# Optimization experiments

Measured on AMD Instinct MI355X. Metric: run time of the kernel, lower is better.

Reference implementation:

```python
import jax, jax.numpy as jnp
import numpy as np

B, S, D = 4, 2048, 512
H, DK, DV = 8, 64, 64
DFF = 2048
LN_EPS = 1e-5


def _layernorm(x, g, b):
    mu = jnp.mean(x, axis=-1, keepdims=True)
    var = jnp.mean(jnp.square(x - mu), axis=-1, keepdims=True)
    return (x - mu) * jax.lax.rsqrt(var + LN_EPS) * g + b


def setup_inputs() -> dict:
    key = jax.random.key(0)
    ks = jax.random.split(key, 9)
    def xavier(k, shape):
        fan_out, fan_in = shape
        std = np.sqrt(2.0 / (fan_in + fan_out))
        return jax.random.normal(k, shape, jnp.float32) * std
    GELU_GAIN = 1.85
    return {
        "x": jax.random.normal(ks[0], (B, S, D), jnp.float32),
        "attention_mask": jax.random.randint(ks[1], (B, S), 0, 2).astype(bool),
        "Wq": xavier(ks[2], (H * DK, D)),
        "Wk": xavier(ks[3], (H * DK, D)),
        "Wv": xavier(ks[4], (H * DV, D)),
        "Wp": xavier(ks[5], (D, H * DV)),
        "W1": xavier(ks[6], (DFF, D)) * GELU_GAIN,
        "b1": jnp.zeros((DFF,), jnp.float32),
        "W2": xavier(ks[7], (D, DFF)),
        "b2": jnp.zeros((D,), jnp.float32),
        "ln1_g": jnp.ones((D,), jnp.float32),
        "ln1_b": jnp.zeros((D,), jnp.float32),
        "ln2_g": jnp.ones((D,), jnp.float32),
        "ln2_b": jnp.zeros((D,), jnp.float32),
    }


def reference(x, attention_mask, Wq, Wk, Wv, Wp, W1, b1, W2, b2,
              ln1_g, ln1_b, ln2_g, ln2_b):
    b, s, d = x.shape
    residual = x
    q = (x @ Wq.T).reshape(b, s, H, DK)  # [B,S,H,DK]
    k = (x @ Wk.T).reshape(b, s, H, DK)
    v = (x @ Wv.T).reshape(b, s, H, DV)
    score = jnp.einsum("bshd,bthd->bhst", q, k) * (DK ** -0.5)  # [B,H,S,S]
    # subtractive mask: score -= 100 * not(mask)
    score = score - 100.0 * (~attention_mask)[:, None, None, :].astype(score.dtype)
    p = jax.nn.softmax(score, axis=-1)
    ctx = jnp.einsum("bhst,bthd->bshd", p, v).reshape(b, s, H * DV)
    att = ctx @ Wp.T  # dropout p=0.1 is identity in eval
    h = _layernorm(att + residual, ln1_g, ln1_b)
    ff = jax.nn.gelu(h @ W1.T + b1, approximate=False) @ W2.T + b2
    out = _layernorm(ff + h, ln2_g, ln2_b)
    return out
```

## Files before the change

kernel.cpp:

```cpp
#include <hip/hip_runtime.h>
#include <cstdint>
#include <cstddef>

#define B_ 4
#define S_ 2048
#define D_ 512
#define H_ 8
#define DK_ 64
#define DFF_ 2048

using s16x8  = __attribute__((ext_vector_type(8))) short;
using bf16x8 = __attribute__((ext_vector_type(8))) __bf16;
using f32x4  = __attribute__((ext_vector_type(4))) float;

__device__ __forceinline__ short f2bf(float f) {
  unsigned u = __builtin_bit_cast(unsigned, f);
  u += 0x7FFFu + ((u >> 16) & 1u);
  return (short)(u >> 16);
}
__device__ __forceinline__ float bf2f(short s) {
  unsigned u = ((unsigned)(unsigned short)s) << 16;
  return __builtin_bit_cast(float, u);
}

__device__ __forceinline__ void gl2lds16(const void* g, void* l) {
  __builtin_amdgcn_global_load_lds(
      (const __attribute__((address_space(1))) void*)g,
      (__attribute__((address_space(3))) void*)l, 16, 0, 0);
}

__global__ __launch_bounds__(256)
void cvt_all(const float* __restrict__ x, const float* __restrict__ Wq,
             const float* __restrict__ Wk, const float* __restrict__ Wv,
             const float* __restrict__ Wp, const float* __restrict__ W1,
             const float* __restrict__ W2,
             short* __restrict__ xb, short* __restrict__ wqkv,
             short* __restrict__ wp, short* __restrict__ w1, short* __restrict__ w2) {
  int blk = blockIdx.x;
  const float* src; short* dst; int off;
  if (blk < 4096)      { src = x;  dst = xb;            off = blk; }
  else if (blk < 4352) { src = Wq; dst = wqkv;          off = blk - 4096; }
  else if (blk < 4608) { src = Wk; dst = wqkv + 262144; off = blk - 4352; }
  else if (blk < 4864) { src = Wv; dst = wqkv + 524288; off = blk - 4608; }
  else if (blk < 5120) { src = Wp; dst = wp;            off = blk - 4864; }
  else if (blk < 6144) { src = W1; dst = w1;            off = blk - 5120; }
  else                 { src = W2; dst = w2;            off = blk - 6144; }
  int i = (off * 256 + threadIdx.x) * 4;
  float4 v = *(const float4*)(src + i);
  *(short4*)(dst + i) = make_short4(f2bf(v.x), f2bf(v.y), f2bf(v.z), f2bf(v.w));
}

__global__ __launch_bounds__(256) void mask_detect(const unsigned* __restrict__ m,
                                                   unsigned* __restrict__ flag) {
  int i = blockIdx.x * 256 + threadIdx.x;
  unsigned v = m[i];
  if (v) atomicOr(flag, v);
}

__global__ __launch_bounds__(256) void mask_convert(const void* __restrict__ m,
                                                    const unsigned* __restrict__ flag,
                                                    float* __restrict__ mb) {
  int i = blockIdx.x * 256 + threadIdx.x;
  unsigned f = *flag;
  int v;
  if ((f & ~1u) == 0u)            v = ((const int*)m)[i];
  else if (f == 0x3F800000u)      v = (((const float*)m)[i] != 0.0f);
  else                            v = ((const unsigned char*)m)[i];
  mb[i] = v ? 0.0f : -100.0f;
}

constexpr int BM = 128, BN = 128, BK = 32;

template <int MODE>
__global__ __launch_bounds__(256)
void gemm_bt(const short* __restrict__ A, const short* __restrict__ B,
             int M, int N, int K,
             const float* __restrict__ aux1,
             void* __restrict__ out0, void* __restrict__ out1, void* __restrict__ out2) {
  __shared__ alignas(16) short As[BM][BK];
  __shared__ alignas(16) short Bs[BN][BK];

  const int tid  = threadIdx.x;
  const int lane = tid & 63;
  const int wave = tid >> 6;
  const int quad = lane >> 4;
  const int l16  = lane & 15;
  const int wm   = (wave >> 1) * 64;
  const int wn   = (wave & 1) * 64;
  const int bm   = blockIdx.x * BM;
  const int bn   = blockIdx.y * BN;

  const short* Ag = A + (size_t)(bm + wave * 32 + (lane >> 2)) * K + (lane & 3) * 8;
  const short* Bg = B + (size_t)(bn + wave * 32 + (lane >> 2)) * K + (lane & 3) * 8;
  short* AsW = &As[wave * 32][0];
  short* BsW = &Bs[wave * 32][0];
  const size_t row16 = (size_t)16 * K;

  f32x4 acc[4][4] = {};

  for (int k0 = 0; k0 < K; k0 += BK) {
    gl2lds16(Ag + k0,          AsW);
    gl2lds16(Ag + k0 + row16,  AsW + 16 * BK);
    gl2lds16(Bg + k0,          BsW);
    gl2lds16(Bg + k0 + row16,  BsW + 16 * BK);
    __syncthreads();

    bf16x8 a[4], b[4];
#pragma unroll
    for (int i = 0; i < 4; ++i)
      a[i] = __builtin_bit_cast(bf16x8, *(const s16x8*)&As[wm + i * 16 + l16][quad * 8]);
#pragma unroll
    for (int j = 0; j < 4; ++j)
      b[j] = __builtin_bit_cast(bf16x8, *(const s16x8*)&Bs[wn + j * 16 + l16][quad * 8]);
#pragma unroll
    for (int i = 0; i < 4; ++i)
#pragma unroll
      for (int j = 0; j < 4; ++j)
        acc[i][j] = __builtin_amdgcn_mfma_f32_16x16x32_bf16(a[i], b[j], acc[i][j], 0, 0, 0);
    __syncthreads();
  }

#pragma unroll
  for (int i = 0; i < 4; ++i) {
    const int m0 = bm + wm + i * 16 + quad * 4;
#pragma unroll
    for (int j = 0; j < 4; ++j) {
      const int n = bn + wn + j * 16 + l16;
      if constexpr (MODE == 0) {
        const int bb = m0 >> 11, ss0 = m0 & 2047;
        if (n >= 1024) {
          const int nn = n - 1024;
          short4 pk = make_short4(f2bf(acc[i][j][0]), f2bf(acc[i][j][1]),
                                  f2bf(acc[i][j][2]), f2bf(acc[i][j][3]));
          *(short4*)((short*)out2 +
              ((((size_t)bb * H_ + (nn >> 6)) * 64 + (nn & 63)) * S_ + ss0)) = pk;
        } else {
          short* dst = (n < 512) ? (short*)out0 : (short*)out1;
          const float sc_ = (n < 512) ? 0.125f : 1.0f;
          const int hh = (n >> 6) & 7, dd = n & 63;
          const size_t rowb = ((size_t)bb * H_ + hh) * S_ + ss0;
#pragma unroll
          for (int rr = 0; rr < 4; ++rr)
            dst[(rowb + rr) * 64 + dd] = f2bf(acc[i][j][rr] * sc_);
        }
      } else {
#pragma unroll
        for (int rr = 0; rr < 4; ++rr) {
          float t = acc[i][j][rr] + aux1[n];
          float gl = 0.5f * t * (1.0f + erff(t * 0.70710678118f));
          ((short*)out0)[(size_t)(m0 + rr) * N + n] = f2bf(gl);
        }
      }
    }
  }
}

template <int MODE>
__global__ __launch_bounds__(128)
void gemm_bt2(const short* __restrict__ A, const short* __restrict__ B,
              int M, int N, int K,
              const float* __restrict__ aux1, const short* __restrict__ auxb,
              float* __restrict__ out0) {
  __shared__ alignas(16) short As[128][32];
  __shared__ alignas(16) short Bs[64][32];

  const int tid  = threadIdx.x;
  const int lane = tid & 63;
  const int wave = tid >> 6;
  const int quad = lane >> 4;
  const int l16  = lane & 15;
  const int wm   = wave * 64;
  const int bm   = blockIdx.x * 128;
  const int bn   = blockIdx.y * 64;

  const int srow = wave * 16 + (lane >> 2);
  const int scol = (lane & 3) * 8;
  const short* Ag = A + (size_t)(bm + srow) * K + scol;
  const short* Bg = B + (size_t)(bn + srow) * K + scol;
  short* AsW = &As[wave * 16][0];
  short* BsW = &Bs[wave * 16][0];
  const size_t row32 = (size_t)32 * K;

  f32x4 acc[4][4] = {};

  for (int k0 = 0; k0 < K; k0 += 32) {
    gl2lds16(Ag + k0,              AsW);
    gl2lds16(Ag + k0 + row32,      AsW + 32 * 32);
    gl2lds16(Ag + k0 + 2 * row32,  AsW + 64 * 32);
    gl2lds16(Ag + k0 + 3 * row32,  AsW + 96 * 32);
    gl2lds16(Bg + k0,              BsW);
    gl2lds16(Bg + k0 + row32,      BsW + 32 * 32);
    __syncthreads();

    bf16x8 a[4], b[4];
#pragma unroll
    for (int i = 0; i < 4; ++i)
      a[i] = __builtin_bit_cast(bf16x8, *(const s16x8*)&As[wm + i * 16 + l16][quad * 8]);
#pragma unroll
    for (int j = 0; j < 4; ++j)
      b[j] = __builtin_bit_cast(bf16x8, *(const s16x8*)&Bs[j * 16 + l16][quad * 8]);
#pragma unroll
    for (int i = 0; i < 4; ++i)
#pragma unroll
      for (int j = 0; j < 4; ++j)
        acc[i][j] = __builtin_amdgcn_mfma_f32_16x16x32_bf16(a[i], b[j], acc[i][j], 0, 0, 0);
    __syncthreads();
  }

#pragma unroll
  for (int i = 0; i < 4; ++i) {
    const int m0 = bm + wm + i * 16 + quad * 4;
#pragma unroll
    for (int j = 0; j < 4; ++j) {
      const int n = bn + j * 16 + l16;
#pragma unroll
      for (int rr = 0; rr < 4; ++rr) {
        float v = acc[i][j][rr];
        if constexpr (MODE == 1) {
          out0[(size_t)(m0 + rr) * N + n] = v + aux1[(size_t)(m0 + rr) * N + n];
        } else {
          out0[(size_t)(m0 + rr) * N + n] =
              v + aux1[n] + bf2f(auxb[(size_t)(m0 + rr) * N + n]);
        }
      }
    }
  }
}

__global__ __launch_bounds__(256)
void flash_attn_mfma(const short* __restrict__ Qb, const short* __restrict__ Kb,
                     const short* __restrict__ Vtg, const float* __restrict__ maskbias,
                     short* __restrict__ ctxb) {
  __shared__ alignas(16) short Ks[64][72];
  __shared__ alignas(16) short Vt[64][72];
  __shared__ alignas(16) short Ps[4][32][72];
  __shared__ alignas(16) float mrow[S_];

  const int b = blockIdx.z, h = blockIdx.y;
  const int tid = threadIdx.x;
  const int w = tid >> 6, lane = tid & 63;
  const int quad = lane >> 4, l16 = lane & 15;
  const size_t base  = ((size_t)(b * H_ + h)) * S_ * DK_;
  const size_t baseT = ((size_t)(b * H_ + h)) * DK_ * S_;
  const int q0 = blockIdx.x * 128;

  {
    const float4* mp = (const float4*)(maskbias + (size_t)b * S_);
    ((float4*)mrow)[tid]       = mp[tid];
    ((float4*)mrow)[tid + 256] = mp[tid + 256];
  }

  bf16x8 qa[2][2];
#pragma unroll
  for (int st = 0; st < 2; ++st) {
    const short* qp = Qb + base + (size_t)(q0 + w * 32 + st * 16 + l16) * 64 + quad * 8;
    qa[st][0] = __builtin_bit_cast(bf16x8, *(const s16x8*)(qp));
    qa[st][1] = __builtin_bit_cast(bf16x8, *(const s16x8*)(qp + 32));
  }

  f32x4 Oc[2][4] = {};
  float li[2][4] = {};

  const int r = tid >> 2, c16 = (tid & 3) * 16;
  const short* kp = Kb  + base  + (size_t)r * 64 + c16;
  const short* vp = Vtg + baseT + (size_t)r * S_ + c16;

  s16x8 kr0 = *(const s16x8*)(kp);
  s16x8 kr1 = *(const s16x8*)(kp + 8);
  s16x8 vr0 = *(const s16x8*)(vp);
  s16x8 vr1 = *(const s16x8*)(vp + 8);

  for (int t0 = 0; t0 < S_; t0 += 64) {
    __syncthreads();
    *(s16x8*)&Ks[r][c16]     = kr0;
    *(s16x8*)&Ks[r][c16 + 8] = kr1;
    *(s16x8*)&Vt[r][c16]     = vr0;
    *(s16x8*)&Vt[r][c16 + 8] = vr1;
    __syncthreads();

    if (t0 + 64 < S_) {
      kr0 = *(const s16x8*)(kp + (size_t)(t0 + 64) * 64);
      kr1 = *(const s16x8*)(kp + (size_t)(t0 + 64) * 64 + 8);
      vr0 = *(const s16x8*)(vp + t0 + 64);
      vr1 = *(const s16x8*)(vp + t0 + 64 + 8);
    }

    f32x4 sc[2][4] = {};
#pragma unroll
    for (int c = 0; c < 2; ++c) {
#pragma unroll
      for (int jt = 0; jt < 4; ++jt) {
        bf16x8 kb = __builtin_bit_cast(bf16x8,
            *(const s16x8*)&Ks[jt * 16 + l16][c * 32 + quad * 8]);
        sc[0][jt] = __builtin_amdgcn_mfma_f32_16x16x32_bf16(qa[0][c], kb, sc[0][jt], 0, 0, 0);
        sc[1][jt] = __builtin_amdgcn_mfma_f32_16x16x32_bf16(qa[1][c], kb, sc[1][jt], 0, 0, 0);
      }
    }

    float mb4[4];
#pragma unroll
    for (int jt = 0; jt < 4; ++jt) mb4[jt] = mrow[t0 + jt * 16 + l16];
#pragma unroll
    for (int st = 0; st < 2; ++st) {
#pragma unroll
      for (int jt = 0; jt < 4; ++jt) {
#pragma unroll
        for (int rr = 0; rr < 4; ++rr) {
          float p = __expf(sc[st][jt][rr] + mb4[jt]);
          unsigned u = __builtin_bit_cast(unsigned, p) & 0xFFFF0000u;
          li[st][rr] += __builtin_bit_cast(float, u);
          Ps[w][st * 16 + quad * 4 + rr][jt * 16 + l16] = (short)(u >> 16);
        }
      }
    }

#pragma unroll
    for (int c = 0; c < 2; ++c) {
      bf16x8 pa0 = __builtin_bit_cast(bf16x8,
          *(const s16x8*)&Ps[w][l16][c * 32 + quad * 8]);
      bf16x8 pa1 = __builtin_bit_cast(bf16x8,
          *(const s16x8*)&Ps[w][16 + l16][c * 32 + quad * 8]);
#pragma unroll
      for (int dt = 0; dt < 4; ++dt) {
        bf16x8 vb = __builtin_bit_cast(bf16x8,
            *(const s16x8*)&Vt[dt * 16 + l16][c * 32 + quad * 8]);
        Oc[0][dt] = __builtin_amdgcn_mfma_f32_16x16x32_bf16(pa0, vb, Oc[0][dt], 0, 0, 0);
        Oc[1][dt] = __builtin_amdgcn_mfma_f32_16x16x32_bf16(pa1, vb, Oc[1][dt], 0, 0, 0);
      }
    }
  }

#pragma unroll
  for (int st = 0; st < 2; ++st) {
#pragma unroll
    for (int rr = 0; rr < 4; ++rr) {
      float l = li[st][rr];
#pragma unroll
      for (int m = 1; m < 16; m <<= 1) l += __shfl_xor(l, m);
      float inv = 1.f / l;
      const size_t row = (size_t)b * S_ + q0 + w * 32 + st * 16 + quad * 4 + rr;
#pragma unroll
      for (int dt = 0; dt < 4; ++dt)
        ctxb[row * (H_ * DK_) + h * 64 + dt * 16 + l16] = f2bf(Oc[st][dt][rr] * inv);
    }
  }
}

__global__ __launch_bounds__(256)
void ln_kernel(const float* __restrict__ y, const float* __restrict__ g,
               const float* __restrict__ bb, float* __restrict__ out32,
               short* __restrict__ outb) {
  const int wave = threadIdx.x >> 6, lane = threadIdx.x & 63;
  const int token = blockIdx.x * 4 + wave;
  const float* row = y + (size_t)token * D_;
  float4 v0 = *(const float4*)(row + lane * 8);
  float4 v1 = *(const float4*)(row + lane * 8 + 4);
  float sum = v0.x + v0.y + v0.z + v0.w + v1.x + v1.y + v1.z + v1.w;
#pragma unroll
  for (int m = 1; m < 64; m <<= 1) sum += __shfl_xor(sum, m);
  float mu = sum * (1.0f / D_);
  float d0 = v0.x - mu, d1 = v0.y - mu, d2 = v0.z - mu, d3 = v0.w - mu;
  float d4 = v1.x - mu, d5 = v1.y - mu, d6 = v1.z - mu, d7 = v1.w - mu;
  float vs = d0*d0 + d1*d1 + d2*d2 + d3*d3 + d4*d4 + d5*d5 + d6*d6 + d7*d7;
#pragma unroll
  for (int m = 1; m < 64; m <<= 1) vs += __shfl_xor(vs, m);
  float rstd = rsqrtf(vs * (1.0f / D_) + 1e-5f);
  float o[8] = {d0, d1, d2, d3, d4, d5, d6, d7};
  int c = lane * 8;
#pragma unroll
  for (int i = 0; i < 8; ++i) {
    float val = o[i] * rstd * g[c + i] + bb[c + i];
    if (out32) out32[(size_t)token * D_ + c + i] = val;
    if (outb)  outb[(size_t)token * D_ + c + i] = f2bf(val);
  }
}

constexpr size_t OFF_XB   = 0;
constexpr size_t OFF_WQKV = 8388608;
constexpr size_t OFF_WP   = 9961472;
constexpr size_t OFF_W1   = 10485760;
constexpr size_t OFF_W2   = 12582912;
constexpr size_t OFF_Q    = 14680064;
constexpr size_t OFF_K    = 23068672;
constexpr size_t OFF_VT   = 31457280;
constexpr size_t OFF_CTX  = 39845888;
constexpr size_t OFF_Y1   = 48234496;
constexpr size_t OFF_HB   = 81788928;
constexpr size_t OFF_FF1  = 14680064;
constexpr size_t OFF_Y2   = 48234496;
constexpr size_t OFF_MB   = 90177536;
constexpr size_t OFF_FLAG = 90210304;
constexpr size_t WS_NEED  = 90210308;

extern "C" void kernel_launch(void* const* d_in, const int* in_sizes, int n_in,
                              void* d_out, int out_size, void* d_ws, size_t ws_size,
                              hipStream_t stream) {
  if (ws_size < WS_NEED) return;

  const float* x    = (const float*)d_in[0];
  const void*  msk  = d_in[1];
  const float* Wq   = (const float*)d_in[2];
  const float* Wk   = (const float*)d_in[3];
  const float* Wv   = (const float*)d_in[4];
  const float* Wp   = (const float*)d_in[5];
  const float* W1   = (const float*)d_in[6];
  const float* b1   = (const float*)d_in[7];
  const float* W2   = (const float*)d_in[8];
  const float* b2   = (const float*)d_in[9];
  const float* ln1g = (const float*)d_in[10];
  const float* ln1b = (const float*)d_in[11];
  const float* ln2g = (const float*)d_in[12];
  const float* ln2b = (const float*)d_in[13];

  char* ws = (char*)d_ws;
  short* xb    = (short*)(ws + OFF_XB);
  short* wqkv  = (short*)(ws + OFF_WQKV);
  short* Wpb   = (short*)(ws + OFF_WP);
  short* W1b   = (short*)(ws + OFF_W1);
  short* W2b   = (short*)(ws + OFF_W2);
  short* Qbh   = (short*)(ws + OFF_Q);
  short* Kbh   = (short*)(ws + OFF_K);
  short* VTb   = (short*)(ws + OFF_VT);
  short* ctxb  = (short*)(ws + OFF_CTX);
  float* y1    = (float*)(ws + OFF_Y1);
  short* hb    = (short*)(ws + OFF_HB);
  short* ff1b  = (short*)(ws + OFF_FF1);
  float* y2    = (float*)(ws + OFF_Y2);
  float* mbias = (float*)(ws + OFF_MB);
  unsigned* flag = (unsigned*)(ws + OFF_FLAG);

  hipMemsetAsync(flag, 0, 4, stream);
  mask_detect<<<8, 256, 0, stream>>>((const unsigned*)msk, flag);
  mask_convert<<<32, 256, 0, stream>>>(msk, flag, mbias);

  cvt_all<<<7168, 256, 0, stream>>>(x, Wq, Wk, Wv, Wp, W1, W2,
                                    xb, wqkv, Wpb, W1b, W2b);

  gemm_bt<0><<<dim3(64, 12), 256, 0, stream>>>(xb, wqkv, 8192, 1536, 512,
                                               nullptr, Qbh, Kbh, VTb);

  flash_attn_mfma<<<dim3(S_ / 128, H_, B_), 256, 0, stream>>>(Qbh, Kbh, VTb, mbias, ctxb);

  gemm_bt2<1><<<dim3(64, 8), 128, 0, stream>>>(ctxb, Wpb, 8192, 512, 512,
                                               x, nullptr, y1);

  ln_kernel<<<2048, 256, 0, stream>>>(y1, ln1g, ln1b, nullptr, hb);

  gemm_bt<2><<<dim3(64, 16), 256, 0, stream>>>(hb, W1b, 8192, 2048, 512,
                                               b1, ff1b, nullptr, nullptr);

  gemm_bt2<3><<<dim3(64, 8), 128, 0, stream>>>(ff1b, W2b, 8192, 512, 2048,
                                               b2, hb, y2);

  ln_kernel<<<2048, 256, 0, stream>>>(y2, ln2g, ln2b, (float*)d_out, nullptr);
}
```

Measured before the change: 342.6 us.

## Use 2-wave attention blocks with 64 query rows per wave, store Q transposed

The flash attention kernel now runs 128 threads per block, and each wave handles 64 query rows instead of 32. Each K/V tile loaded into shared memory is therefore reused across more MFMAs per wave, and staging moves to 4 vectors per thread. The QKV GEMM epilogue now writes Q transposed with packed short4 stores (same layout as V), and the attention kernel gathers Q with scalar strided loads. This adds register pressure (launch bounds 128,1), halves the waves per block, and makes the one-time Q load uncoalesced.

```diff
diff --git a/kernel.cpp b/kernel.cpp
--- a/kernel.cpp
+++ b/kernel.cpp
@@ -128,20 +128,24 @@
       const int n = bn + wn + j * 16 + l16;
       if constexpr (MODE == 0) {
         const int bb = m0 >> 11, ss0 = m0 & 2047;
-        if (n >= 1024) {
+        if (n < 512) {
+          short4 pk = make_short4(f2bf(acc[i][j][0] * 0.125f), f2bf(acc[i][j][1] * 0.125f),
+                                  f2bf(acc[i][j][2] * 0.125f), f2bf(acc[i][j][3] * 0.125f));
+          *(short4*)((short*)out0 +
+              ((((size_t)bb * H_ + (n >> 6)) * 64 + (n & 63)) * S_ + ss0)) = pk;
+        } else if (n >= 1024) {
           const int nn = n - 1024;
           short4 pk = make_short4(f2bf(acc[i][j][0]), f2bf(acc[i][j][1]),
                                   f2bf(acc[i][j][2]), f2bf(acc[i][j][3]));
           *(short4*)((short*)out2 +
               ((((size_t)bb * H_ + (nn >> 6)) * 64 + (nn & 63)) * S_ + ss0)) = pk;
         } else {
-          short* dst = (n < 512) ? (short*)out0 : (short*)out1;
-          const float sc_ = (n < 512) ? 0.125f : 1.0f;
-          const int hh = (n >> 6) & 7, dd = n & 63;
+          const int nn = n - 512;
+          const int hh = nn >> 6, dd = nn & 63;
           const size_t rowb = ((size_t)bb * H_ + hh) * S_ + ss0;
 #pragma unroll
           for (int rr = 0; rr < 4; ++rr)
-            dst[(rowb + rr) * 64 + dd] = f2bf(acc[i][j][rr] * sc_);
+            ((short*)out1)[(rowb + rr) * 64 + dd] = f2bf(acc[i][j][rr]);
         }
       } else {
 #pragma unroll
@@ -227,13 +231,13 @@
   }
 }
 
-__global__ __launch_bounds__(256)
-void flash_attn_mfma(const short* __restrict__ Qb, const short* __restrict__ Kb,
+__global__ __launch_bounds__(128, 1)
+void flash_attn_mfma(const short* __restrict__ QTg, const short* __restrict__ Kb,
                      const short* __restrict__ Vtg, const float* __restrict__ maskbias,
                      short* __restrict__ ctxb) {
   __shared__ alignas(16) short Ks[64][72];
   __shared__ alignas(16) short Vt[64][72];
-  __shared__ alignas(16) short Ps[4][32][72];
+  __shared__ alignas(16) short Ps[2][64][72];
   __shared__ alignas(16) float mrow[S_];
 
   const int b = blockIdx.z, h = blockIdx.y;
@@ -246,54 +250,65 @@
 
   {
     const float4* mp = (const float4*)(maskbias + (size_t)b * S_);
-    ((float4*)mrow)[tid]       = mp[tid];
-    ((float4*)mrow)[tid + 256] = mp[tid + 256];
-  }
-
-  bf16x8 qa[2][2];
-#pragma unroll
-  for (int st = 0; st < 2; ++st) {
-    const short* qp = Qb + base + (size_t)(q0 + w * 32 + st * 16 + l16) * 64 + quad * 8;
-    qa[st][0] = __builtin_bit_cast(bf16x8, *(const s16x8*)(qp));
-    qa[st][1] = __builtin_bit_cast(bf16x8, *(const s16x8*)(qp + 32));
-  }
-
-  f32x4 Oc[2][4] = {};
-  float li[2][4] = {};
-
-  const int r = tid >> 2, c16 = (tid & 3) * 16;
-  const short* kp = Kb  + base  + (size_t)r * 64 + c16;
-  const short* vp = Vtg + baseT + (size_t)r * S_ + c16;
-
-  s16x8 kr0 = *(const s16x8*)(kp);
-  s16x8 kr1 = *(const s16x8*)(kp + 8);
-  s16x8 vr0 = *(const s16x8*)(vp);
-  s16x8 vr1 = *(const s16x8*)(vp + 8);
+#pragma unroll
+    for (int i = 0; i < 4; ++i) ((float4*)mrow)[tid + i * 128] = mp[tid + i * 128];
+  }
+
+  bf16x8 qa[4][2];
+#pragma unroll
+  for (int st = 0; st < 4; ++st) {
+    const int q = q0 + w * 64 + st * 16 + l16;
+#pragma unroll
+    for (int c = 0; c < 2; ++c) {
+      s16x8 t;
+#pragma unroll
+      for (int j = 0; j < 8; ++j)
+        t[j] = QTg[baseT + (size_t)(c * 32 + quad * 8 + j) * S_ + q];
+      qa[st][c] = __builtin_bit_cast(bf16x8, t);
+    }
+  }
+
+  f32x4 Oc[4][4] = {};
+  float li[4][4] = {};
+
+  const int r = tid >> 1, c32 = (tid & 1) * 32;
+  const short* kp = Kb  + base  + (size_t)r * 64 + c32;
+  const short* vp = Vtg + baseT + (size_t)r * S_ + c32;
+
+  s16x8 kr[4], vr[4];
+#pragma unroll
+  for (int u = 0; u < 4; ++u) {
+    kr[u] = *(const s16x8*)(kp + u * 8);
+    vr[u] = *(const s16x8*)(vp + u * 8);
+  }
 
   for (int t0 = 0; t0 < S_; t0 += 64) {
     __syncthreads();
-    *(s16x8*)&Ks[r][c16]     = kr0;
-    *(s16x8*)&Ks[r][c16 + 8] = kr1;
-    *(s16x8*)&Vt[r][c16]     = vr0;
-    *(s16x8*)&Vt[r][c16 + 8] = vr1;
+#pragma unroll
+    for (int u = 0; u < 4; ++u) {
+      *(s16x8*)&Ks[r][c32 + u * 8] = kr[u];
+      *(s16x8*)&Vt[r][c32 + u * 8] = vr[u];
+    }
     __syncthreads();
 
     if (t0 + 64 < S_) {
-      kr0 = *(const s16x8*)(kp + (size_t)(t0 + 64) * 64);
-      kr1 = *(const s16x8*)(kp + (size_t)(t0 + 64) * 64 + 8);
-      vr0 = *(const s16x8*)(vp + t0 + 64);
-      vr1 = *(const s16x8*)(vp + t0 + 64 + 8);
-    }
-
-    f32x4 sc[2][4] = {};
+#pragma unroll
+      for (int u = 0; u < 4; ++u) {
+        kr[u] = *(const s16x8*)(kp + (size_t)(t0 + 64) * 64 + u * 8);
+        vr[u] = *(const s16x8*)(vp + (t0 + 64) + u * 8);
+      }
+    }
+
+    f32x4 sc[4][4] = {};
 #pragma unroll
     for (int c = 0; c < 2; ++c) {
 #pragma unroll
       for (int jt = 0; jt < 4; ++jt) {
         bf16x8 kb = __builtin_bit_cast(bf16x8,
             *(const s16x8*)&Ks[jt * 16 + l16][c * 32 + quad * 8]);
-        sc[0][jt] = __builtin_amdgcn_mfma_f32_16x16x32_bf16(qa[0][c], kb, sc[0][jt], 0, 0, 0);
-        sc[1][jt] = __builtin_amdgcn_mfma_f32_16x16x32_bf16(qa[1][c], kb, sc[1][jt], 0, 0, 0);
+#pragma unroll
+        for (int st = 0; st < 4; ++st)
+          sc[st][jt] = __builtin_amdgcn_mfma_f32_16x16x32_bf16(qa[st][c], kb, sc[st][jt], 0, 0, 0);
       }
     }
 
@@ -301,7 +316,7 @@
 #pragma unroll
     for (int jt = 0; jt < 4; ++jt) mb4[jt] = mrow[t0 + jt * 16 + l16];
 #pragma unroll
-    for (int st = 0; st < 2; ++st) {
+    for (int st = 0; st < 4; ++st) {
 #pragma unroll
       for (int jt = 0; jt < 4; ++jt) {
 #pragma unroll
@@ -316,29 +331,31 @@
 
 #pragma unroll
     for (int c = 0; c < 2; ++c) {
-      bf16x8 pa0 = __builtin_bit_cast(bf16x8,
-          *(const s16x8*)&Ps[w][l16][c * 32 + quad * 8]);
-      bf16x8 pa1 = __builtin_bit_cast(bf16x8,
-          *(const s16x8*)&Ps[w][16 + l16][c * 32 + quad * 8]);
+      bf16x8 pa[4];
+#pragma unroll
+      for (int st = 0; st < 4; ++st)
+        pa[st] = __builtin_bit_cast(bf16x8,
+            *(const s16x8*)&Ps[w][st * 16 + l16][c * 32 + quad * 8]);
 #pragma unroll
       for (int dt = 0; dt < 4; ++dt) {
         bf16x8 vb = __builtin_bit_cast(bf16x8,
             *(const s16x8*)&Vt[dt * 16 + l16][c * 32 + quad * 8]);
-        Oc[0][dt] = __builtin_amdgcn_mfma_f32_16x16x32_bf16(pa0, vb, Oc[0][dt], 0, 0, 0);
-        Oc[1][dt] = __builtin_amdgcn_mfma_f32_16x16x32_bf16(pa1, vb, Oc[1][dt], 0, 0, 0);
-      }
-    }
-  }
-
-#pragma unroll
-  for (int st = 0; st < 2; ++st) {
+#pragma unroll
+        for (int st = 0; st < 4; ++st)
+          Oc[st][dt] = __builtin_amdgcn_mfma_f32_16x16x32_bf16(pa[st], vb, Oc[st][dt], 0, 0, 0);
+      }
+    }
+  }
+
+#pragma unroll
+  for (int st = 0; st < 4; ++st) {
 #pragma unroll
     for (int rr = 0; rr < 4; ++rr) {
       float l = li[st][rr];
 #pragma unroll
       for (int m = 1; m < 16; m <<= 1) l += __shfl_xor(l, m);
       float inv = 1.f / l;
-      const size_t row = (size_t)b * S_ + q0 + w * 32 + st * 16 + quad * 4 + rr;
+      const size_t row = (size_t)b * S_ + q0 + w * 64 + st * 16 + quad * 4 + rr;
 #pragma unroll
       for (int dt = 0; dt < 4; ++dt)
         ctxb[row * (H_ * DK_) + h * 64 + dt * 16 + l16] = f2bf(Oc[st][dt][rr] * inv);
@@ -380,7 +397,7 @@
 constexpr size_t OFF_WP   = 9961472;
 constexpr size_t OFF_W1   = 10485760;
 constexpr size_t OFF_W2   = 12582912;
-constexpr size_t OFF_Q    = 14680064;
+constexpr size_t OFF_QT   = 14680064;
 constexpr size_t OFF_K    = 23068672;
 constexpr size_t OFF_VT   = 31457280;
 constexpr size_t OFF_CTX  = 39845888;
@@ -418,7 +435,7 @@
   short* Wpb   = (short*)(ws + OFF_WP);
   short* W1b   = (short*)(ws + OFF_W1);
   short* W2b   = (short*)(ws + OFF_W2);
-  short* Qbh   = (short*)(ws + OFF_Q);
+  short* QTb   = (short*)(ws + OFF_QT);
   short* Kbh   = (short*)(ws + OFF_K);
   short* VTb   = (short*)(ws + OFF_VT);
   short* ctxb  = (short*)(ws + OFF_CTX);
@@ -437,9 +454,9 @@
                                     xb, wqkv, Wpb, W1b, W2b);
 
   gemm_bt<0><<<dim3(64, 12), 256, 0, stream>>>(xb, wqkv, 8192, 1536, 512,
-                                               nullptr, Qbh, Kbh, VTb);
-
-  flash_attn_mfma<<<dim3(S_ / 128, H_, B_), 256, 0, stream>>>(Qbh, Kbh, VTb, mbias, ctxb);
+                                               nullptr, QTb, Kbh, VTb);
+
+  flash_attn_mfma<<<dim3(S_ / 128, H_, B_), 128, 0, stream>>>(QTb, Kbh, VTb, mbias, ctxb);
 
   gemm_bt2<1><<<dim3(64, 8), 128, 0, stream>>>(ctxb, Wpb, 8192, 512, 512,
                                                x, nullptr, y1);
```

After: 347.9 us. No clear change (+1.5%).

## Split-K the N=512 GEMMs and fuse residual/bias adds into layernorm

Applied to the files above, without the earlier changes.

The two 512-wide output GEMMs now run with split-K over two z-slices, each writing raw fp32 partials. A fused layernorm kernel sums the partials and adds the residual (x or h) and bias before normalizing. This doubles the block count for the small-N GEMMs to fill more CUs, at the cost of extra fp32 partial traffic. Q is also stored transposed (d-major), like K-side V, so the QKV epilogue writes packed short4 stores, while flash attention gathers Q with strided scalar loads.

```diff
diff --git a/kernel.cpp b/kernel.cpp
--- a/kernel.cpp
+++ b/kernel.cpp
@@ -128,20 +128,24 @@
       const int n = bn + wn + j * 16 + l16;
       if constexpr (MODE == 0) {
         const int bb = m0 >> 11, ss0 = m0 & 2047;
-        if (n >= 1024) {
+        if (n < 512) {
+          short4 pk = make_short4(f2bf(acc[i][j][0] * 0.125f), f2bf(acc[i][j][1] * 0.125f),
+                                  f2bf(acc[i][j][2] * 0.125f), f2bf(acc[i][j][3] * 0.125f));
+          *(short4*)((short*)out0 +
+              ((((size_t)bb * H_ + (n >> 6)) * 64 + (n & 63)) * S_ + ss0)) = pk;
+        } else if (n >= 1024) {
           const int nn = n - 1024;
           short4 pk = make_short4(f2bf(acc[i][j][0]), f2bf(acc[i][j][1]),
                                   f2bf(acc[i][j][2]), f2bf(acc[i][j][3]));
           *(short4*)((short*)out2 +
               ((((size_t)bb * H_ + (nn >> 6)) * 64 + (nn & 63)) * S_ + ss0)) = pk;
         } else {
-          short* dst = (n < 512) ? (short*)out0 : (short*)out1;
-          const float sc_ = (n < 512) ? 0.125f : 1.0f;
-          const int hh = (n >> 6) & 7, dd = n & 63;
+          const int nn = n - 512;
+          const int hh = nn >> 6, dd = nn & 63;
           const size_t rowb = ((size_t)bb * H_ + hh) * S_ + ss0;
 #pragma unroll
           for (int rr = 0; rr < 4; ++rr)
-            dst[(rowb + rr) * 64 + dd] = f2bf(acc[i][j][rr] * sc_);
+            ((short*)out1)[(rowb + rr) * 64 + dd] = f2bf(acc[i][j][rr]);
         }
       } else {
 #pragma unroll
@@ -155,12 +159,9 @@
   }
 }
 
-template <int MODE>
 __global__ __launch_bounds__(128)
-void gemm_bt2(const short* __restrict__ A, const short* __restrict__ B,
-              int M, int N, int K,
-              const float* __restrict__ aux1, const short* __restrict__ auxb,
-              float* __restrict__ out0) {
+void gemm_bt2_sk(const short* __restrict__ A, const short* __restrict__ B,
+                 int M, int N, int K, float* __restrict__ outp) {
   __shared__ alignas(16) short As[128][32];
   __shared__ alignas(16) short Bs[64][32];
 
@@ -172,18 +173,20 @@
   const int wm   = wave * 64;
   const int bm   = blockIdx.x * 128;
   const int bn   = blockIdx.y * 64;
+  const int Kh   = K >> 1;
+  const int koff = blockIdx.z * Kh;
 
   const int srow = wave * 16 + (lane >> 2);
   const int scol = (lane & 3) * 8;
-  const short* Ag = A + (size_t)(bm + srow) * K + scol;
-  const short* Bg = B + (size_t)(bn + srow) * K + scol;
+  const short* Ag = A + (size_t)(bm + srow) * K + koff + scol;
+  const short* Bg = B + (size_t)(bn + srow) * K + koff + scol;
   short* AsW = &As[wave * 16][0];
   short* BsW = &Bs[wave * 16][0];
   const size_t row32 = (size_t)32 * K;
 
   f32x4 acc[4][4] = {};
 
-  for (int k0 = 0; k0 < K; k0 += 32) {
+  for (int k0 = 0; k0 < Kh; k0 += 32) {
     gl2lds16(Ag + k0,              AsW);
     gl2lds16(Ag + k0 + row32,      AsW + 32 * 32);
     gl2lds16(Ag + k0 + 2 * row32,  AsW + 64 * 32);
@@ -207,6 +210,7 @@
     __syncthreads();
   }
 
+  float* dst = outp + (size_t)blockIdx.z * M * N;
 #pragma unroll
   for (int i = 0; i < 4; ++i) {
     const int m0 = bm + wm + i * 16 + quad * 4;
@@ -214,21 +218,14 @@
     for (int j = 0; j < 4; ++j) {
       const int n = bn + j * 16 + l16;
 #pragma unroll
-      for (int rr = 0; rr < 4; ++rr) {
-        float v = acc[i][j][rr];
-        if constexpr (MODE == 1) {
-          out0[(size_t)(m0 + rr) * N + n] = v + aux1[(size_t)(m0 + rr) * N + n];
-        } else {
-          out0[(size_t)(m0 + rr) * N + n] =
-              v + aux1[n] + bf2f(auxb[(size_t)(m0 + rr) * N + n]);
-        }
-      }
+      for (int rr = 0; rr < 4; ++rr)
+        dst[(size_t)(m0 + rr) * N + n] = acc[i][j][rr];
     }
   }
 }
 
 __global__ __launch_bounds__(256)
-void flash_attn_mfma(const short* __restrict__ Qb, const short* __restrict__ Kb,
+void flash_attn_mfma(const short* __restrict__ QTg, const short* __restrict__ Kb,
                      const short* __restrict__ Vtg, const float* __restrict__ maskbias,
                      short* __restrict__ ctxb) {
   __shared__ alignas(16) short Ks[64][72];
@@ -253,9 +250,15 @@
   bf16x8 qa[2][2];
 #pragma unroll
   for (int st = 0; st < 2; ++st) {
-    const short* qp = Qb + base + (size_t)(q0 + w * 32 + st * 16 + l16) * 64 + quad * 8;
-    qa[st][0] = __builtin_bit_cast(bf16x8, *(const s16x8*)(qp));
-    qa[st][1] = __builtin_bit_cast(bf16x8, *(const s16x8*)(qp + 32));
+    const int q = q0 + w * 32 + st * 16 + l16;
+#pragma unroll
+    for (int c = 0; c < 2; ++c) {
+      s16x8 t;
+#pragma unroll
+      for (int j = 0; j < 8; ++j)
+        t[j] = QTg[baseT + (size_t)(c * 32 + quad * 8 + j) * S_ + q];
+      qa[st][c] = __builtin_bit_cast(bf16x8, t);
+    }
   }
 
   f32x4 Oc[2][4] = {};
@@ -347,31 +350,61 @@
 }
 
 __global__ __launch_bounds__(256)
-void ln_kernel(const float* __restrict__ y, const float* __restrict__ g,
-               const float* __restrict__ bb, float* __restrict__ out32,
-               short* __restrict__ outb) {
+void ln_fused(const float* __restrict__ p0, const float* __restrict__ p1,
+              const float* __restrict__ xres, const short* __restrict__ hres,
+              const float* __restrict__ bias,
+              const float* __restrict__ g, const float* __restrict__ bb,
+              float* __restrict__ out32, short* __restrict__ outb) {
   const int wave = threadIdx.x >> 6, lane = threadIdx.x & 63;
   const int token = blockIdx.x * 4 + wave;
-  const float* row = y + (size_t)token * D_;
-  float4 v0 = *(const float4*)(row + lane * 8);
-  float4 v1 = *(const float4*)(row + lane * 8 + 4);
-  float sum = v0.x + v0.y + v0.z + v0.w + v1.x + v1.y + v1.z + v1.w;
+  const size_t off = (size_t)token * D_;
+  const int c = lane * 8;
+
+  float v[8];
+  {
+    float4 a0 = *(const float4*)(p0 + off + c);
+    float4 a1 = *(const float4*)(p0 + off + c + 4);
+    float4 b0 = *(const float4*)(p1 + off + c);
+    float4 b1 = *(const float4*)(p1 + off + c + 4);
+    v[0]=a0.x+b0.x; v[1]=a0.y+b0.y; v[2]=a0.z+b0.z; v[3]=a0.w+b0.w;
+    v[4]=a1.x+b1.x; v[5]=a1.y+b1.y; v[6]=a1.z+b1.z; v[7]=a1.w+b1.w;
+  }
+  if (xres) {
+    float4 x0 = *(const float4*)(xres + off + c);
+    float4 x1 = *(const float4*)(xres + off + c + 4);
+    v[0]+=x0.x; v[1]+=x0.y; v[2]+=x0.z; v[3]+=x0.w;
+    v[4]+=x1.x; v[5]+=x1.y; v[6]+=x1.z; v[7]+=x1.w;
+  }
+  if (hres) {
+    short4 h0 = *(const short4*)(hres + off + c);
+    short4 h1 = *(const short4*)(hres + off + c + 4);
+    v[0]+=bf2f(h0.x); v[1]+=bf2f(h0.y); v[2]+=bf2f(h0.z); v[3]+=bf2f(h0.w);
+    v[4]+=bf2f(h1.x); v[5]+=bf2f(h1.y); v[6]+=bf2f(h1.z); v[7]+=bf2f(h1.w);
+  }
+  if (bias) {
+    float4 c0 = *(const float4*)(bias + c);
+    float4 c1 = *(const float4*)(bias + c + 4);
+    v[0]+=c0.x; v[1]+=c0.y; v[2]+=c0.z; v[3]+=c0.w;
+    v[4]+=c1.x; v[5]+=c1.y; v[6]+=c1.z; v[7]+=c1.w;
+  }
+
+  float sum = 0.f;
+#pragma unroll
+  for (int i = 0; i < 8; ++i) sum += v[i];
 #pragma unroll
   for (int m = 1; m < 64; m <<= 1) sum += __shfl_xor(sum, m);
   float mu = sum * (1.0f / D_);
-  float d0 = v0.x - mu, d1 = v0.y - mu, d2 = v0.z - mu, d3 = v0.w - mu;
-  float d4 = v1.x - mu, d5 = v1.y - mu, d6 = v1.z - mu, d7 = v1.w - mu;
-  float vs = d0*d0 + d1*d1 + d2*d2 + d3*d3 + d4*d4 + d5*d5 + d6*d6 + d7*d7;
+  float vs = 0.f;
+#pragma unroll
+  for (int i = 0; i < 8; ++i) { v[i] -= mu; vs += v[i] * v[i]; }
 #pragma unroll
   for (int m = 1; m < 64; m <<= 1) vs += __shfl_xor(vs, m);
   float rstd = rsqrtf(vs * (1.0f / D_) + 1e-5f);
-  float o[8] = {d0, d1, d2, d3, d4, d5, d6, d7};
-  int c = lane * 8;
 #pragma unroll
   for (int i = 0; i < 8; ++i) {
-    float val = o[i] * rstd * g[c + i] + bb[c + i];
-    if (out32) out32[(size_t)token * D_ + c + i] = val;
-    if (outb)  outb[(size_t)token * D_ + c + i] = f2bf(val);
+    float val = v[i] * rstd * g[c + i] + bb[c + i];
+    if (out32) out32[off + c + i] = val;
+    if (outb)  outb[off + c + i] = f2bf(val);
   }
 }
 
@@ -380,14 +413,14 @@
 constexpr size_t OFF_WP   = 9961472;
 constexpr size_t OFF_W1   = 10485760;
 constexpr size_t OFF_W2   = 12582912;
-constexpr size_t OFF_Q    = 14680064;
+constexpr size_t OFF_QT   = 14680064;
 constexpr size_t OFF_K    = 23068672;
 constexpr size_t OFF_VT   = 31457280;
 constexpr size_t OFF_CTX  = 39845888;
-constexpr size_t OFF_Y1   = 48234496;
+constexpr size_t OFF_P0   = 48234496;
+constexpr size_t OFF_P1   = 65011712;
 constexpr size_t OFF_HB   = 81788928;
 constexpr size_t OFF_FF1  = 14680064;
-constexpr size_t OFF_Y2   = 48234496;
 constexpr size_t OFF_MB   = 90177536;
 constexpr size_t OFF_FLAG = 90210304;
 constexpr size_t WS_NEED  = 90210308;
@@ -418,14 +451,13 @@
   short* Wpb   = (short*)(ws + OFF_WP);
   short* W1b   = (short*)(ws + OFF_W1);
   short* W2b   = (short*)(ws + OFF_W2);
-  short* Qbh   = (short*)(ws + OFF_Q);
+  short* QTb   = (short*)(ws + OFF_QT);
   short* Kbh   = (short*)(ws + OFF_K);
   short* VTb   = (short*)(ws + OFF_VT);
   short* ctxb  = (short*)(ws + OFF_CTX);
-  float* y1    = (float*)(ws + OFF_Y1);
+  float* p0    = (float*)(ws + OFF_P0);
   short* hb    = (short*)(ws + OFF_HB);
   short* ff1b  = (short*)(ws + OFF_FF1);
-  float* y2    = (float*)(ws + OFF_Y2);
   float* mbias = (float*)(ws + OFF_MB);
   unsigned* flag = (unsigned*)(ws + OFF_FLAG);
 
@@ -437,20 +469,20 @@
                                     xb, wqkv, Wpb, W1b, W2b);
 
   gemm_bt<0><<<dim3(64, 12), 256, 0, stream>>>(xb, wqkv, 8192, 1536, 512,
-                                               nullptr, Qbh, Kbh, VTb);
-
-  flash_attn_mfma<<<dim3(S_ / 128, H_, B_), 256, 0, stream>>>(Qbh, Kbh, VTb, mbias, ctxb);
-
-  gemm_bt2<1><<<dim3(64, 8), 128, 0, stream>>>(ctxb, Wpb, 8192, 512, 512,
-                                               x, nullptr, y1);
-
-  ln_kernel<<<2048, 256, 0, stream>>>(y1, ln1g, ln1b, nullptr, hb);
+                                               nullptr, QTb, Kbh, VTb);
+
+  flash_attn_mfma<<<dim3(S_ / 128, H_, B_), 256, 0, stream>>>(QTb, Kbh, VTb, mbias, ctxb);
+
+  gemm_bt2_sk<<<dim3(64, 8, 2), 128, 0, stream>>>(ctxb, Wpb, 8192, 512, 512, p0);
+
+  ln_fused<<<2048, 256, 0, stream>>>(p0, p0 + (size_t)8192 * 512, x, nullptr, nullptr,
+                                     ln1g, ln1b, nullptr, hb);
 
   gemm_bt<2><<<dim3(64, 16), 256, 0, stream>>>(hb, W1b, 8192, 2048, 512,
                                                b1, ff1b, nullptr, nullptr);
 
-  gemm_bt2<3><<<dim3(64, 8), 128, 0, stream>>>(ff1b, W2b, 8192, 512, 2048,
-                                               b2, hb, y2);
-
-  ln_kernel<<<2048, 256, 0, stream>>>(y2, ln2g, ln2b, (float*)d_out, nullptr);
-}
+  gemm_bt2_sk<<<dim3(64, 8, 2), 128, 0, stream>>>(ff1b, W2b, 8192, 512, 2048, p0);
+
+  ln_fused<<<2048, 256, 0, stream>>>(p0, p0 + (size_t)8192 * 512, nullptr, hb, b2,
+                                     ln2g, ln2b, (float*)d_out, nullptr);
+}
```

Measured after the change: 340.8 us. About the same (-0.5%).
